# Optimization experiments

Hardware: AMD Instinct MI355X
Metric: run time of the kernel (lower is better)

The kernel has to match this reference:

```python
import jax, jax.numpy as jnp
import numpy as np

D_MODEL = 1024
NUM_HEADS = 16
HEAD_DIM = D_MODEL // NUM_HEADS
BATCH, SEQ = 2, 2048


def setup_inputs() -> dict:
    key = jax.random.key(0)
    ks = jax.random.split(key, 5)
    scale = 1.0 / np.sqrt(D_MODEL)  # ~xavier magnitude
    x = jax.random.normal(ks[0], (BATCH, SEQ, D_MODEL), dtype=jnp.float32)
    Wq = jax.random.normal(ks[1], (D_MODEL, D_MODEL), dtype=jnp.float32) * scale
    Wk = jax.random.normal(ks[2], (D_MODEL, D_MODEL), dtype=jnp.float32) * scale
    Wv = jax.random.normal(ks[3], (D_MODEL, D_MODEL), dtype=jnp.float32) * scale
    Wo = jax.random.normal(ks[4], (D_MODEL, D_MODEL), dtype=jnp.float32) * scale
    z = jnp.zeros((D_MODEL,), dtype=jnp.float32)
    return {"x": x, "Wq": Wq, "bq": z, "Wk": Wk, "bk": z, "Wv": Wv, "bv": z, "Wo": Wo, "bo": z}


def reference(x, Wq, bq, Wk, bk, Wv, bv, Wo, bo):
    B, S, _ = x.shape
    H, Dh = NUM_HEADS, HEAD_DIM
    # torch Linear convention: y = x @ W^T + b
    q = (x @ Wq.T + bq).reshape(B, S, H, Dh)
    k = (x @ Wk.T + bk).reshape(B, S, H, Dh)
    v = (x @ Wv.T + bv).reshape(B, S, H, Dh)
    # scores: [B, H, S, S]
    scores = jnp.einsum('bqhd,bkhd->bhqk', q, k) / np.sqrt(Dh).astype(np.float32)
    attn = jax.nn.softmax(scores, axis=-1)
    out = jnp.einsum('bhqk,bkhd->bqhd', attn, v).reshape(B, S, H * Dh)
    return out @ Wo.T + bo
```

## Files before the change

### kernel.cpp

```cpp
#include <hip/hip_runtime.h>
#include <hip/hip_bf16.h>

typedef __bf16 bf16;
typedef __bf16 bf16x8 __attribute__((ext_vector_type(8)));
typedef __bf16 bf16x4 __attribute__((ext_vector_type(4)));
typedef float f32x4 __attribute__((ext_vector_type(4)));

constexpr int DM = 1024, NH = 16, DH = 64, NB = 2, SQ = 2048;
constexpr int MTOT = NB * SQ;
constexpr float QSCALE = 0.125f * 1.44269504088896f;

__device__ __forceinline__ void gld_lds16(const bf16* g, bf16* l) {
  __builtin_amdgcn_global_load_lds(
      (const __attribute__((address_space(1))) void*)g,
      (__attribute__((address_space(3))) void*)l, 16, 0, 0);
}

__global__ __launch_bounds__(256) void cvt5(
    const float* __restrict__ s0, const float* __restrict__ s1,
    const float* __restrict__ s2, const float* __restrict__ s3,
    const float* __restrict__ s4,
    bf16* __restrict__ d0, bf16* __restrict__ d1, bf16* __restrict__ d2,
    bf16* __restrict__ d3, bf16* __restrict__ d4) {
  const int idx = (blockIdx.x * 256 + threadIdx.x) * 4;
  const float* src; bf16* dst; int reps;
  switch (blockIdx.y) {
    case 0: src = s0; dst = d0; reps = 1; break;
    case 1: src = s1; dst = d1; reps = 1; break;
    case 2: src = s2; dst = d2; reps = 1; break;
    case 3: src = s3; dst = d3; reps = 1; break;
    default: src = s4; dst = d4; reps = 4; break;
  }
  for (int j = 0; j < reps; j++) {
    const int o = idx + j * (DM * DM);
    const float4 v = *(const float4*)(src + o);
    *(bf16x4*)(dst + o) = (bf16x4){(bf16)v.x, (bf16)v.y, (bf16)v.z, (bf16)v.w};
  }
}

template <int BM, typename OutT>
__device__ __forceinline__ void gemm_tile(
    const bf16* __restrict__ A, const bf16* __restrict__ Bm,
    const float* __restrict__ bias, OutT* __restrict__ C,
    int rowA0, int rowB0, int N, int K, bool bias_row, float cscale,
    bf16* sA, bf16* sB) {
  constexpr int NT = (BM == 128) ? 4 : 2;
  const int tid = threadIdx.x;
  const int wave = tid >> 6, lane = tid & 63;
  const int quad = lane >> 4, l16 = lane & 15;
  const int row0w = (BM == 128) ? (wave >> 1) * 64 : 0;
  const int col0w = (BM == 128) ? (wave & 1) * 64 : wave * 32;

  f32x4 acc[4][NT];
#pragma unroll
  for (int i = 0; i < 4; i++)
#pragma unroll
    for (int j = 0; j < NT; j++) acc[i][j] = (f32x4){0.f, 0.f, 0.f, 0.f};

  const int srow = lane >> 3;
  const int scol = ((lane & 7) ^ srow) * 8;

  for (int kt = 0; kt < K; kt += 64) {
#pragma unroll
    for (int i = 0; i < BM / 32; i++) {
      const int r = i * 32 + wave * 8;
      gld_lds16(A + (size_t)(rowA0 + r + srow) * K + kt + scol, &sA[r * 64]);
    }
#pragma unroll
    for (int i = 0; i < 4; i++) {
      const int r = i * 32 + wave * 8;
      gld_lds16(Bm + (size_t)(rowB0 + r + srow) * K + kt + scol, &sB[r * 64]);
    }
    __syncthreads();
#pragma unroll
    for (int kk = 0; kk < 64; kk += 32) {
      bf16x8 aF[4], bF[NT];
      const int slot = (((kk >> 3) + quad) ^ (l16 & 7)) << 3;
#pragma unroll
      for (int mt = 0; mt < 4; mt++)
        aF[mt] = *(const bf16x8*)&sA[(row0w + mt * 16 + l16) * 64 + slot];
#pragma unroll
      for (int nt = 0; nt < NT; nt++)
        bF[nt] = *(const bf16x8*)&sB[(col0w + nt * 16 + l16) * 64 + slot];
#pragma unroll
      for (int mt = 0; mt < 4; mt++)
#pragma unroll
        for (int nt = 0; nt < NT; nt++)
          acc[mt][nt] = __builtin_amdgcn_mfma_f32_16x16x32_bf16(aF[mt], bF[nt], acc[mt][nt], 0, 0, 0);
    }
    __syncthreads();
  }

#pragma unroll
  for (int mt = 0; mt < 4; mt++) {
#pragma unroll
    for (int nt = 0; nt < NT; nt++) {
#pragma unroll
      for (int r = 0; r < 4; r++) {
        const int row = rowA0 + row0w + mt * 16 + quad * 4 + r;
        const int col = rowB0 + col0w + nt * 16 + l16;
        const float bb = bias_row ? bias[row] : bias[col];
        C[(size_t)row * N + col] = (OutT)((acc[mt][nt][r] + bb) * cscale);
      }
    }
  }
}

__global__ __launch_bounds__(256, 4) void qkv_gemm(
    const bf16* __restrict__ xb, const bf16* __restrict__ Wqb,
    const bf16* __restrict__ Wkb, const bf16* __restrict__ Wvb,
    const float* __restrict__ bq, const float* __restrict__ bk,
    const float* __restrict__ bv,
    bf16* __restrict__ Qw, bf16* __restrict__ Kw, bf16* __restrict__ VTw) {
  __shared__ alignas(16) bf16 sA[128 * 64];
  __shared__ alignas(16) bf16 sB[128 * 64];
  if (blockIdx.z == 0) {
    gemm_tile<128, bf16>(xb, Wqb, bq, Qw, blockIdx.x * 128, blockIdx.y * 128, DM, DM, false, QSCALE, sA, sB);
  } else if (blockIdx.z == 1) {
    gemm_tile<128, bf16>(xb, Wkb, bk, Kw, blockIdx.x * 128, blockIdx.y * 128, DM, DM, false, 1.0f, sA, sB);
  } else {
    const int id = blockIdx.y * 32 + blockIdx.x;
    gemm_tile<128, bf16>(Wvb, xb, bv, VTw, (id >> 5) * 128, (id & 31) * 128, MTOT, DM, true, 1.0f, sA, sB);
  }
}

__global__ __launch_bounds__(256, 4) void out_gemm(
    const bf16* __restrict__ A, const bf16* __restrict__ Bm,
    const float* __restrict__ bias, float* __restrict__ C) {
  __shared__ alignas(16) bf16 sA[64 * 64];
  __shared__ alignas(16) bf16 sB[128 * 64];
  gemm_tile<64, float>(A, Bm, bias, C, blockIdx.x * 64, blockIdx.y * 128, DM, DM, false, 1.0f, sA, sB);
}

__global__ __launch_bounds__(256, 2) void attn(
    const bf16* __restrict__ Q, const bf16* __restrict__ Kq,
    const bf16* __restrict__ VT, bf16* __restrict__ O) {
  __shared__ alignas(16) bf16 sK[2][128 * 64];
  __shared__ alignas(16) bf16 sV[2][64 * 128];
  __shared__ alignas(16) bf16 sP[4][32 * 64];
  const int tid = threadIdx.x, wave = tid >> 6, lane = tid & 63;
  const int quad = lane >> 4, l16 = lane & 15;
  const int hb = blockIdx.x, qt = blockIdx.y;
  const int h = hb & 15, b = hb >> 4;

  const bf16* Qg = Q + (size_t)(b * SQ + qt * 128) * DM + h * DH;
  const bf16* Kg = Kq + (size_t)(b * SQ) * DM + h * DH;
  const bf16* Vg = VT + (size_t)(h * DH) * MTOT + b * SQ;

  const int srow = lane >> 3, scol = ((lane & 7) ^ srow) * 8;
  const int vrow = lane >> 4;

  auto stageKV = [&](int t, int buf) {
#pragma unroll
    for (int i = 0; i < 4; i++) {
      const int r = (wave * 4 + i) * 8;
      gld_lds16(Kg + (size_t)(t * 128 + r + srow) * DM + scol, &sK[buf][r * 64]);
    }
#pragma unroll
    for (int i = 0; i < 4; i++) {
      const int r = (wave * 4 + i) * 4;
      const int vchunk = (lane & 15) ^ ((r + vrow) & 7);
      gld_lds16(Vg + (size_t)(r + vrow) * MTOT + t * 128 + vchunk * 8, &sV[buf][r * 128]);
    }
  };

  bf16x8 qF[2][2];
#pragma unroll
  for (int mt = 0; mt < 2; mt++)
#pragma unroll
    for (int kkh = 0; kkh < 2; kkh++)
      qF[mt][kkh] = *(const bf16x8*)(Qg + (size_t)(wave * 32 + mt * 16 + l16) * DM +
                                     kkh * 32 + quad * 8);

  float l_i[2] = {0.f, 0.f};
  f32x4 o_acc[2][4];
#pragma unroll
  for (int mt = 0; mt < 2; mt++)
#pragma unroll
    for (int n2 = 0; n2 < 4; n2++) o_acc[mt][n2] = (f32x4){0.f, 0.f, 0.f, 0.f};

  stageKV(0, 0);
  for (int t = 0; t < 16; ++t) {
    __syncthreads();
    if (t + 1 < 16) stageKV(t + 1, (t + 1) & 1);
    const bf16* cK = sK[t & 1];
    const bf16* cV = sV[t & 1];

    f32x4 sacc[2][8];
#pragma unroll
    for (int mt = 0; mt < 2; mt++)
#pragma unroll
      for (int nt = 0; nt < 8; nt++) sacc[mt][nt] = (f32x4){0.f, 0.f, 0.f, 0.f};
#pragma unroll
    for (int kk = 0; kk < 64; kk += 32) {
      bf16x8 kF[8];
      const int slot = (((kk >> 3) + quad) ^ (l16 & 7)) << 3;
#pragma unroll
      for (int nt = 0; nt < 8; nt++)
        kF[nt] = *(const bf16x8*)&cK[(nt * 16 + l16) * 64 + slot];
#pragma unroll
      for (int mt = 0; mt < 2; mt++)
#pragma unroll
        for (int nt = 0; nt < 8; nt++)
          sacc[mt][nt] = __builtin_amdgcn_mfma_f32_16x16x32_bf16(kF[nt], qF[mt][kk >> 5],
                                                                 sacc[mt][nt], 0, 0, 0);
    }

#pragma unroll
    for (int half = 0; half < 2; half++) {
#pragma unroll
      for (int mt = 0; mt < 2; mt++) {
        const int row = mt * 16 + l16;
#pragma unroll
        for (int nt4 = 0; nt4 < 4; nt4++) {
          const f32x4 s = sacc[mt][half * 4 + nt4];
          bf16x4 pk;
#pragma unroll
          for (int r = 0; r < 4; r++) {
            const float p = __builtin_amdgcn_exp2f(s[r]);
            l_i[mt] += p;
            pk[r] = (bf16)p;
          }
          const int c = 2 * nt4 + (quad >> 1);
          *(bf16x4*)&sP[wave][row * 64 + ((c ^ (row & 7)) << 3) + (quad & 1) * 4] = pk;
        }
      }
#pragma unroll
      for (int kk = 0; kk < 64; kk += 32) {
        bf16x8 pF[2], vF[4];
#pragma unroll
        for (int mt = 0; mt < 2; mt++) {
          const int row = mt * 16 + l16;
          const int c = (kk >> 3) + quad;
          pF[mt] = *(const bf16x8*)&sP[wave][row * 64 + ((c ^ (row & 7)) << 3)];
        }
#pragma unroll
        for (int n2 = 0; n2 < 4; n2++) {
          const int ch = ((half * 64 + kk) >> 3) + quad;
          vF[n2] = *(const bf16x8*)&cV[(n2 * 16 + l16) * 128 + ((ch ^ (l16 & 7)) << 3)];
        }
#pragma unroll
        for (int mt = 0; mt < 2; mt++)
#pragma unroll
          for (int n2 = 0; n2 < 4; n2++)
            o_acc[mt][n2] = __builtin_amdgcn_mfma_f32_16x16x32_bf16(pF[mt], vF[n2],
                                                                    o_acc[mt][n2], 0, 0, 0);
      }
    }
  }

  float* lbuf = (float*)&sP[wave][0];
#pragma unroll
  for (int mt = 0; mt < 2; mt++) {
    float v = l_i[mt];
    v += __shfl_xor(v, 16);
    v += __shfl_xor(v, 32);
    if (quad == 0) lbuf[mt * 16 + l16] = v;
  }
  __builtin_amdgcn_s_waitcnt(0);
#pragma unroll
  for (int mt = 0; mt < 2; mt++) {
    const f32x4 lv = *(const f32x4*)&lbuf[mt * 16 + quad * 4];
#pragma unroll
    for (int r = 0; r < 4; r++) {
      const float inv = 1.0f / lv[r];
      const int row = qt * 128 + wave * 32 + mt * 16 + quad * 4 + r;
#pragma unroll
      for (int n2 = 0; n2 < 4; n2++) {
        const int col = n2 * 16 + l16;
        O[(size_t)(b * SQ + row) * DM + h * DH + col] = (bf16)(o_acc[mt][n2][r] * inv);
      }
    }
  }
}

extern "C" void kernel_launch(void* const* d_in, const int* in_sizes, int n_in,
                              void* d_out, int out_size, void* d_ws, size_t ws_size,
                              hipStream_t stream) {
  const float* x  = (const float*)d_in[0];
  const float* Wq = (const float*)d_in[1];
  const float* bq = (const float*)d_in[2];
  const float* Wk = (const float*)d_in[3];
  const float* bk = (const float*)d_in[4];
  const float* Wv = (const float*)d_in[5];
  const float* bv = (const float*)d_in[6];
  const float* Wo = (const float*)d_in[7];
  const float* bo = (const float*)d_in[8];
  float* out = (float*)d_out;

  bf16* ws   = (bf16*)d_ws;
  bf16* xb   = ws;
  bf16* Wqb  = ws + (size_t)MTOT * DM;
  bf16* Wkb  = Wqb + (size_t)DM * DM;
  bf16* Wvb  = Wkb + (size_t)DM * DM;
  bf16* Wob  = Wvb + (size_t)DM * DM;
  bf16* Qw   = Wob + (size_t)DM * DM;
  bf16* Kw   = Qw + (size_t)MTOT * DM;
  bf16* VTw  = Kw + (size_t)MTOT * DM;
  bf16* Cw   = VTw + (size_t)MTOT * DM;

  const dim3 blk(256);
  cvt5<<<dim3(1024, 5), blk, 0, stream>>>(Wq, Wk, Wv, Wo, x,
                                          Wqb, Wkb, Wvb, Wob, xb);
  qkv_gemm<<<dim3(32, 8, 3), blk, 0, stream>>>(xb, Wqb, Wkb, Wvb, bq, bk, bv, Qw, Kw, VTw);
  attn<<<dim3(NH * NB, SQ / 128), blk, 0, stream>>>(Qw, Kw, VTw, Cw);
  out_gemm<<<dim3(MTOT / 64, DM / 128), blk, 0, stream>>>(Cw, Wob, bo, out);
}
```

Before: 184.7 us.

## Split attention waves across query and key halves with cross-wave reduction

The attention kernel now arranges its four waves as 2 query groups by 2 key groups. Each wave handles 64 query rows against half of every 128-key tile, so every K/V fragment loaded from LDS feeds more MFMAs. Partial outputs and row sums are combined through shared memory at the end. The activation conversion is also spread over more blocks instead of looping inside one, which removes load imbalance. The trade-off is more accumulator registers per wave and an extra LDS reduction step.

```diff
diff --git a/kernel.cpp b/kernel.cpp
--- a/kernel.cpp
+++ b/kernel.cpp
@@ -23,19 +23,19 @@
     bf16* __restrict__ d0, bf16* __restrict__ d1, bf16* __restrict__ d2,
     bf16* __restrict__ d3, bf16* __restrict__ d4) {
   const int idx = (blockIdx.x * 256 + threadIdx.x) * 4;
-  const float* src; bf16* dst; int reps;
+  const float* src; bf16* dst;
   switch (blockIdx.y) {
-    case 0: src = s0; dst = d0; reps = 1; break;
-    case 1: src = s1; dst = d1; reps = 1; break;
-    case 2: src = s2; dst = d2; reps = 1; break;
-    case 3: src = s3; dst = d3; reps = 1; break;
-    default: src = s4; dst = d4; reps = 4; break;
-  }
-  for (int j = 0; j < reps; j++) {
-    const int o = idx + j * (DM * DM);
-    const float4 v = *(const float4*)(src + o);
-    *(bf16x4*)(dst + o) = (bf16x4){(bf16)v.x, (bf16)v.y, (bf16)v.z, (bf16)v.w};
-  }
+    case 0: src = s0; dst = d0; break;
+    case 1: src = s1; dst = d1; break;
+    case 2: src = s2; dst = d2; break;
+    case 3: src = s3; dst = d3; break;
+    default: {
+      const int off = (blockIdx.y - 4) * (DM * DM);
+      src = s4 + off; dst = d4 + off; break;
+    }
+  }
+  const float4 v = *(const float4*)(src + idx);
+  *(bf16x4*)(dst + idx) = (bf16x4){(bf16)v.x, (bf16)v.y, (bf16)v.z, (bf16)v.w};
 }
 
 template <int BM, typename OutT>
@@ -137,9 +137,10 @@
     const bf16* __restrict__ VT, bf16* __restrict__ O) {
   __shared__ alignas(16) bf16 sK[2][128 * 64];
   __shared__ alignas(16) bf16 sV[2][64 * 128];
-  __shared__ alignas(16) bf16 sP[4][32 * 64];
+  __shared__ alignas(16) bf16 sP[4][64 * 32];
   const int tid = threadIdx.x, wave = tid >> 6, lane = tid & 63;
   const int quad = lane >> 4, l16 = lane & 15;
+  const int qg = wave >> 1, kg = wave & 1;
   const int hb = blockIdx.x, qt = blockIdx.y;
   const int h = hb & 15, b = hb >> 4;
 
@@ -164,18 +165,18 @@
     }
   };
 
-  bf16x8 qF[2][2];
-#pragma unroll
-  for (int mt = 0; mt < 2; mt++)
+  bf16x8 qF[4][2];
+#pragma unroll
+  for (int mt = 0; mt < 4; mt++)
 #pragma unroll
     for (int kkh = 0; kkh < 2; kkh++)
-      qF[mt][kkh] = *(const bf16x8*)(Qg + (size_t)(wave * 32 + mt * 16 + l16) * DM +
+      qF[mt][kkh] = *(const bf16x8*)(Qg + (size_t)(qg * 64 + mt * 16 + l16) * DM +
                                      kkh * 32 + quad * 8);
 
-  float l_i[2] = {0.f, 0.f};
-  f32x4 o_acc[2][4];
-#pragma unroll
-  for (int mt = 0; mt < 2; mt++)
+  float l_i[4] = {0.f, 0.f, 0.f, 0.f};
+  f32x4 o_acc[4][4];
+#pragma unroll
+  for (int mt = 0; mt < 4; mt++)
 #pragma unroll
     for (int n2 = 0; n2 < 4; n2++) o_acc[mt][n2] = (f32x4){0.f, 0.f, 0.f, 0.f};
 
@@ -186,34 +187,34 @@
     const bf16* cK = sK[t & 1];
     const bf16* cV = sV[t & 1];
 
-    f32x4 sacc[2][8];
-#pragma unroll
-    for (int mt = 0; mt < 2; mt++)
-#pragma unroll
-      for (int nt = 0; nt < 8; nt++) sacc[mt][nt] = (f32x4){0.f, 0.f, 0.f, 0.f};
+    f32x4 sacc[4][4];
+#pragma unroll
+    for (int nt = 0; nt < 4; nt++)
+#pragma unroll
+      for (int mt = 0; mt < 4; mt++) sacc[nt][mt] = (f32x4){0.f, 0.f, 0.f, 0.f};
 #pragma unroll
     for (int kk = 0; kk < 64; kk += 32) {
-      bf16x8 kF[8];
+      bf16x8 kF[4];
       const int slot = (((kk >> 3) + quad) ^ (l16 & 7)) << 3;
 #pragma unroll
-      for (int nt = 0; nt < 8; nt++)
-        kF[nt] = *(const bf16x8*)&cK[(nt * 16 + l16) * 64 + slot];
-#pragma unroll
-      for (int mt = 0; mt < 2; mt++)
-#pragma unroll
-        for (int nt = 0; nt < 8; nt++)
-          sacc[mt][nt] = __builtin_amdgcn_mfma_f32_16x16x32_bf16(kF[nt], qF[mt][kk >> 5],
-                                                                 sacc[mt][nt], 0, 0, 0);
-    }
-
-#pragma unroll
-    for (int half = 0; half < 2; half++) {
-#pragma unroll
-      for (int mt = 0; mt < 2; mt++) {
+      for (int nt = 0; nt < 4; nt++)
+        kF[nt] = *(const bf16x8*)&cK[(kg * 64 + nt * 16 + l16) * 64 + slot];
+#pragma unroll
+      for (int nt = 0; nt < 4; nt++)
+#pragma unroll
+        for (int mt = 0; mt < 4; mt++)
+          sacc[nt][mt] = __builtin_amdgcn_mfma_f32_16x16x32_bf16(kF[nt], qF[mt][kk >> 5],
+                                                                 sacc[nt][mt], 0, 0, 0);
+    }
+
+#pragma unroll
+    for (int kq = 0; kq < 2; kq++) {
+#pragma unroll
+      for (int mt = 0; mt < 4; mt++) {
         const int row = mt * 16 + l16;
 #pragma unroll
-        for (int nt4 = 0; nt4 < 4; nt4++) {
-          const f32x4 s = sacc[mt][half * 4 + nt4];
+        for (int ntl = 0; ntl < 2; ntl++) {
+          const f32x4 s = sacc[kq * 2 + ntl][mt];
           bf16x4 pk;
 #pragma unroll
           for (int r = 0; r < 4; r++) {
@@ -221,54 +222,69 @@
             l_i[mt] += p;
             pk[r] = (bf16)p;
           }
-          const int c = 2 * nt4 + (quad >> 1);
-          *(bf16x4*)&sP[wave][row * 64 + ((c ^ (row & 7)) << 3) + (quad & 1) * 4] = pk;
+          const int c = ntl * 2 + (quad >> 1);
+          *(bf16x4*)&sP[wave][row * 32 + ((c ^ (row & 3)) << 3) + (quad & 1) * 4] = pk;
         }
       }
-#pragma unroll
-      for (int kk = 0; kk < 64; kk += 32) {
-        bf16x8 pF[2], vF[4];
-#pragma unroll
-        for (int mt = 0; mt < 2; mt++) {
-          const int row = mt * 16 + l16;
-          const int c = (kk >> 3) + quad;
-          pF[mt] = *(const bf16x8*)&sP[wave][row * 64 + ((c ^ (row & 7)) << 3)];
-        }
-#pragma unroll
-        for (int n2 = 0; n2 < 4; n2++) {
-          const int ch = ((half * 64 + kk) >> 3) + quad;
-          vF[n2] = *(const bf16x8*)&cV[(n2 * 16 + l16) * 128 + ((ch ^ (l16 & 7)) << 3)];
-        }
-#pragma unroll
-        for (int mt = 0; mt < 2; mt++)
-#pragma unroll
-          for (int n2 = 0; n2 < 4; n2++)
-            o_acc[mt][n2] = __builtin_amdgcn_mfma_f32_16x16x32_bf16(pF[mt], vF[n2],
-                                                                    o_acc[mt][n2], 0, 0, 0);
+      bf16x8 pF[4], vF[4];
+#pragma unroll
+      for (int mt = 0; mt < 4; mt++) {
+        const int row = mt * 16 + l16;
+        pF[mt] = *(const bf16x8*)&sP[wave][row * 32 + ((quad ^ (row & 3)) << 3)];
       }
-    }
-  }
-
-  float* lbuf = (float*)&sP[wave][0];
-#pragma unroll
-  for (int mt = 0; mt < 2; mt++) {
+      const int chbase = kg * 8 + kq * 4;
+#pragma unroll
+      for (int n2 = 0; n2 < 4; n2++)
+        vF[n2] = *(const bf16x8*)&cV[(n2 * 16 + l16) * 128 +
+                                     (((chbase + quad) ^ (l16 & 7)) << 3)];
+#pragma unroll
+      for (int mt = 0; mt < 4; mt++)
+#pragma unroll
+        for (int n2 = 0; n2 < 4; n2++)
+          o_acc[mt][n2] = __builtin_amdgcn_mfma_f32_16x16x32_bf16(pF[mt], vF[n2],
+                                                                  o_acc[mt][n2], 0, 0, 0);
+    }
+  }
+
+  __syncthreads();
+  float* obuf = (float*)&sK[0][0];
+  float* lb   = (float*)&sV[0][0];
+  float lred[4];
+#pragma unroll
+  for (int mt = 0; mt < 4; mt++) {
     float v = l_i[mt];
     v += __shfl_xor(v, 16);
     v += __shfl_xor(v, 32);
-    if (quad == 0) lbuf[mt * 16 + l16] = v;
-  }
-  __builtin_amdgcn_s_waitcnt(0);
-#pragma unroll
-  for (int mt = 0; mt < 2; mt++) {
-    const f32x4 lv = *(const f32x4*)&lbuf[mt * 16 + quad * 4];
-#pragma unroll
-    for (int r = 0; r < 4; r++) {
-      const float inv = 1.0f / lv[r];
-      const int row = qt * 128 + wave * 32 + mt * 16 + quad * 4 + r;
-#pragma unroll
-      for (int n2 = 0; n2 < 4; n2++) {
-        const int col = n2 * 16 + l16;
-        O[(size_t)(b * SQ + row) * DM + h * DH + col] = (bf16)(o_acc[mt][n2][r] * inv);
+    lred[mt] = v;
+  }
+  if (quad == 0)
+#pragma unroll
+    for (int mt = 0; mt < 4; mt++) lb[(qg * 2 + kg) * 64 + mt * 16 + l16] = lred[mt];
+  if (kg == 1) {
+#pragma unroll
+    for (int mt = 0; mt < 4; mt++)
+#pragma unroll
+      for (int n2 = 0; n2 < 4; n2++)
+#pragma unroll
+        for (int r = 0; r < 4; r++)
+          obuf[qg * 4096 + (mt * 16 + quad * 4 + r) * 64 + n2 * 16 + l16] = o_acc[mt][n2][r];
+  }
+  __syncthreads();
+  if (kg == 0) {
+#pragma unroll
+    for (int mt = 0; mt < 4; mt++) {
+      const f32x4 l0 = *(const f32x4*)&lb[(qg * 2 + 0) * 64 + mt * 16 + quad * 4];
+      const f32x4 l1 = *(const f32x4*)&lb[(qg * 2 + 1) * 64 + mt * 16 + quad * 4];
+#pragma unroll
+      for (int r = 0; r < 4; r++) {
+        const float inv = 1.0f / (l0[r] + l1[r]);
+        const int row = qt * 128 + qg * 64 + mt * 16 + quad * 4 + r;
+#pragma unroll
+        for (int n2 = 0; n2 < 4; n2++) {
+          const float o = o_acc[mt][n2][r] +
+                          obuf[qg * 4096 + (mt * 16 + quad * 4 + r) * 64 + n2 * 16 + l16];
+          O[(size_t)(b * SQ + row) * DM + h * DH + n2 * 16 + l16] = (bf16)(o * inv);
+        }
       }
     }
   }
@@ -300,7 +316,7 @@
   bf16* Cw   = VTw + (size_t)MTOT * DM;
 
   const dim3 blk(256);
-  cvt5<<<dim3(1024, 5), blk, 0, stream>>>(Wq, Wk, Wv, Wo, x,
+  cvt5<<<dim3(1024, 8), blk, 0, stream>>>(Wq, Wk, Wv, Wo, x,
                                           Wqb, Wkb, Wvb, Wob, xb);
   qkv_gemm<<<dim3(32, 8, 3), blk, 0, stream>>>(xb, Wqb, Wkb, Wvb, bq, bk, bv, Qw, Kw, VTw);
   attn<<<dim3(NH * NB, SQ / 128), blk, 0, stream>>>(Qw, Kw, VTw, Cw);
```

Result: no change. 182.1 us (-1.4%).
